# Optimization experiments

Hardware: AMD Instinct MI355X
Metric: run time of the kernel (lower is better)

## Reference

```python
import jax, jax.numpy as jnp
import numpy as np

F_FRAMES = 128   # number of frames (seq_start_end rows)
P_PEDS = 32      # pedestrians per frame (uniform)
B = F_FRAMES * P_PEDS
E, H, BN, PM, M = 64, 128, 1024, 512, 1024
PRED_LEN = 12


def setup_inputs() -> dict:
    key = jax.random.key(0)
    ks = jax.random.split(key, 20)
    n = lambda k, s, sc=0.05: (jax.random.normal(k, s) * sc).astype(jnp.float32)
    starts = jnp.arange(F_FRAMES, dtype=jnp.int32) * P_PEDS
    seq_start_end = jnp.stack([starts, starts + P_PEDS], axis=1)
    return {
        "h0": n(ks[0], (1, B, H), 1.0),
        "c0": n(ks[1], (1, B, H), 1.0),
        "obs_final_pos": n(ks[2], (B, 2), 1.0),
        "obs_final_pos_rel": n(ks[3], (B, 2), 1.0),
        "W_emb": n(ks[4], (2, E)), "b_emb": jnp.zeros((E,), jnp.float32),
        "W_ih": n(ks[5], (4 * H, E)), "W_hh": n(ks[6], (4 * H, H)),
        "b_ih": jnp.zeros((4 * H,), jnp.float32), "b_hh": jnp.zeros((4 * H,), jnp.float32),
        "W_pos": n(ks[7], (H, 2)), "b_pos": jnp.zeros((2,), jnp.float32),
        "W_pe": n(ks[8], (2, E)), "b_pe": jnp.zeros((E,), jnp.float32),
        "W_p1": n(ks[9], (E + H, PM)), "b_p1": jnp.zeros((PM,), jnp.float32),
        "W_p2": n(ks[10], (PM, BN)), "b_p2": jnp.zeros((BN,), jnp.float32),
        "W_m1": n(ks[11], (H + BN, M)), "b_m1": jnp.zeros((M,), jnp.float32),
        "W_m2": n(ks[12], (M, H)), "b_m2": jnp.zeros((H,), jnp.float32),
        "seq_start_end": seq_start_end,
    }


def reference(h0, c0, obs_final_pos, obs_final_pos_rel,
              W_emb, b_emb, W_ih, W_hh, b_ih, b_hh, W_pos, b_pos,
              W_pe, b_pe, W_p1, b_p1, W_p2, b_p2, W_m1, b_m1, W_m2, b_m2,
              seq_start_end):
    Bn = h0.shape[1]
    F = seq_start_end.shape[0]
    P = Bn // F  # uniform frame size
    h, c = h0[0], c0[0]
    x0 = obs_final_pos_rel @ W_emb + b_emb  # decoder input embedding

    def step(carry, _):
        x, h, c, last_pos = carry
        # LSTM cell (PyTorch gate order i,f,g,o)
        gates = x @ W_ih.T + h @ W_hh.T + b_ih + b_hh  # (B, 4H)
        i, f, g, o = jnp.split(gates, 4, axis=-1)
        i, f, o = jax.nn.sigmoid(i), jax.nn.sigmoid(f), jax.nn.sigmoid(o)
        c_new = f * c + i * jnp.tanh(g)
        h_new = o * jnp.tanh(c_new)
        rel_pos = h_new @ W_pos + b_pos
        curr_pos = rel_pos + last_pos
        # PoolNet: per-frame pairwise rel-pos embed + MLP + max over neighbours j
        pos = curr_pos.reshape(F, P, 2)
        hf = h_new.reshape(F, P, H)
        rel = pos[:, None, :, :] - pos[:, :, None, :]  # rel[f,i,j] = pos_j - pos_i
        e = rel @ W_pe + b_pe  # (F,P,P,E)
        feat = jnp.concatenate(
            [e, jnp.broadcast_to(hf[:, None], (F, P, P, H))], axis=-1)  # h of j
        z = jax.nn.relu(feat @ W_p1 + b_p1)
        z = jax.nn.relu(z @ W_p2 + b_p2)  # (F,P,P,BN)
        pool_h = z.max(axis=2).reshape(Bn, BN)
        # hidden refresh MLP
        mi = jnp.concatenate([h_new, pool_h], axis=-1)
        nh = jax.nn.relu(mi @ W_m1 + b_m1)
        nh = jax.nn.relu(nh @ W_m2 + b_m2)
        x_new = rel_pos @ W_emb + b_emb
        return (x_new, nh, c_new, curr_pos), (curr_pos, rel_pos)

    _, (pred_seq, pred_seq_rel) = jax.lax.scan(
        jax.checkpoint(step), (x0, h, c, obs_final_pos), None, length=PRED_LEN)
    return pred_seq, pred_seq_rel
```

## Files before the change

### kernel.cpp

```cpp
#include <hip/hip_runtime.h>

#define NB 4096
#define HD 128
#define ED 64
#define NF 128
#define NP 32
#define TSTEPS 12

typedef __attribute__((ext_vector_type(8))) short short8;
typedef __attribute__((ext_vector_type(8))) __bf16 bf16x8;
typedef __attribute__((ext_vector_type(8))) _Float16 f16x8;
typedef __attribute__((ext_vector_type(4))) float f32x4;

#define MFMA16(a, b, c) __builtin_amdgcn_mfma_f32_16x16x32_bf16((a), (b), (c), 0, 0, 0)
#define MFMAH(a, b, c)  __builtin_amdgcn_mfma_f32_16x16x32_f16((a), (b), (c), 0, 0, 0)

__device__ __forceinline__ unsigned short f2bf(float f) {
  unsigned int x = __float_as_uint(f);
  x += 0x7fffu + ((x >> 16) & 1u);
  return (unsigned short)(x >> 16);
}

__device__ __forceinline__ float sigm(float x) { return 1.0f / (1.0f + expf(-x)); }

__device__ __forceinline__ f16x8 relu8(f16x8 x) {
  return __builtin_elementwise_max(x, (f16x8)(_Float16)0);
}


__global__ __launch_bounds__(256) void k_transpose_bf(const float* __restrict__ W,
                                                      unsigned short* __restrict__ Wt,
                                                      int K, int N) {
  __shared__ float t[32][33];
  int nb = blockIdx.x * 32, kb = blockIdx.y * 32;
  int tx = threadIdx.x & 31, ty = threadIdx.x >> 5;
  #pragma unroll
  for (int r = 0; r < 32; r += 8)
    t[ty + r][tx] = W[(size_t)(kb + ty + r) * N + nb + tx];
  __syncthreads();
  #pragma unroll
  for (int r = 0; r < 32; r += 8)
    Wt[(size_t)(nb + ty + r) * K + kb + tx] = f2bf(t[tx][ty + r]);
}

__global__ __launch_bounds__(256) void k_pack_bfrag(const float* __restrict__ Wp2,
                                                    _Float16* __restrict__ Bf) {
  int U = blockIdx.x * 256 + threadIdx.x;
  int l = U & 63, cb = (U >> 6) & 63, ks = U >> 12;
  int col = cb * 16 + (l & 15);
  int k0 = ks * 32 + (l >> 4) * 8;
  f16x8 r;
  #pragma unroll
  for (int e = 0; e < 8; ++e) r[e] = (_Float16)Wp2[(size_t)(k0 + e) * 1024 + col];
  *(f16x8*)(Bf + (size_t)U * 8) = r;
}

__global__ __launch_bounds__(256) void k_pack_lstm_w(const float* __restrict__ Wih,
                                                     const float* __restrict__ Whh,
                                                     float* __restrict__ WihT,
                                                     float* __restrict__ WhhT) {
  int idx = blockIdx.x * 256 + threadIdx.x;
  if (idx < 64 * 512) { int k = idx >> 9, n = idx & 511; WihT[idx] = Wih[n * 64 + k]; }
  if (idx < 128 * 512) { int k = idx >> 9, n = idx & 511; WhhT[idx] = Whh[n * 128 + k]; }
}

__global__ __launch_bounds__(256) void k_pack_wpp(const float* __restrict__ Wpe,
                                                  const float* __restrict__ bpe,
                                                  const float* __restrict__ Wp1,
                                                  const float* __restrict__ bp1,
                                                  float* __restrict__ Wpp,
                                                  float* __restrict__ cvec) {
  int n = blockIdx.x * 256 + threadIdx.x;
  if (n >= 512) return;
  float s0 = 0.f, s1 = 0.f, sc = 0.f;
  for (int k = 0; k < 64; ++k) {
    float w = Wp1[k * 512 + n];
    s0 += Wpe[k] * w;
    s1 += Wpe[64 + k] * w;
    sc += bpe[k] * w;
  }
  Wpp[n * 2] = s0; Wpp[n * 2 + 1] = s1; cvec[n] = sc + bp1[n];
}

__global__ __launch_bounds__(256) void k_x0(const float* __restrict__ ofr,
                                            const float* __restrict__ Wemb,
                                            const float* __restrict__ bemb,
                                            float* __restrict__ x) {
  int idx = blockIdx.x * 256 + threadIdx.x;
  if (idx >= NB * ED) return;
  int row = idx >> 6, e = idx & 63;
  x[idx] = bemb[e] + ofr[row * 2] * Wemb[e] + ofr[row * 2 + 1] * Wemb[64 + e];
}


__global__ __launch_bounds__(256) void k12_lstm_uv(
    const float* __restrict__ x, const float* __restrict__ hin, const float* __restrict__ cin,
    const float* __restrict__ WihT, const float* __restrict__ WhhT,
    const float* __restrict__ bih, const float* __restrict__ bhh,
    const float* __restrict__ Wpos, const float* __restrict__ bpos,
    const float* __restrict__ Wemb, const float* __restrict__ bemb,
    const float* __restrict__ lastpos,
    const float* __restrict__ Wp1, const float* __restrict__ Wpp,
    const float* __restrict__ cvec,
    float* __restrict__ cout, unsigned short* __restrict__ mi,
    float* __restrict__ posout, float* __restrict__ xout,
    float* __restrict__ outc, float* __restrict__ outr,
    _Float16* __restrict__ u16, _Float16* __restrict__ v16) {
  __shared__ float xh[8][192];
  __shared__ float hnl[8][128];
  __shared__ float rp[8][2];
  __shared__ float cp[8][2];
  int tid = threadIdx.x;
  int r0 = blockIdx.x * 8;
  for (int idx = tid; idx < 8 * 192; idx += 256) {
    int r = idx / 192, k = idx % 192;
    xh[r][k] = (k < 64) ? x[(r0 + r) * 64 + k] : hin[(r0 + r) * 128 + (k - 64)];
  }
  __syncthreads();
  int j = tid & 127, rg = tid >> 7;
  float acc0[4], acc1[4], acc2[4], acc3[4];
  {
    float b0 = bih[j] + bhh[j];
    float b1 = bih[128 + j] + bhh[128 + j];
    float b2 = bih[256 + j] + bhh[256 + j];
    float b3 = bih[384 + j] + bhh[384 + j];
    #pragma unroll
    for (int r = 0; r < 4; ++r) { acc0[r] = b0; acc1[r] = b1; acc2[r] = b2; acc3[r] = b3; }
  }
  for (int k = 0; k < 64; ++k) {
    float w0 = WihT[k * 512 + j], w1 = WihT[k * 512 + 128 + j],
          w2 = WihT[k * 512 + 256 + j], w3 = WihT[k * 512 + 384 + j];
    #pragma unroll
    for (int r = 0; r < 4; ++r) {
      float xv = xh[rg * 4 + r][k];
      acc0[r] += w0 * xv; acc1[r] += w1 * xv; acc2[r] += w2 * xv; acc3[r] += w3 * xv;
    }
  }
  for (int k = 0; k < 128; ++k) {
    float w0 = WhhT[k * 512 + j], w1 = WhhT[k * 512 + 128 + j],
          w2 = WhhT[k * 512 + 256 + j], w3 = WhhT[k * 512 + 384 + j];
    #pragma unroll
    for (int r = 0; r < 4; ++r) {
      float hv = xh[rg * 4 + r][64 + k];
      acc0[r] += w0 * hv; acc1[r] += w1 * hv; acc2[r] += w2 * hv; acc3[r] += w3 * hv;
    }
  }
  #pragma unroll
  for (int r = 0; r < 4; ++r) {
    int row = r0 + rg * 4 + r;
    float ig = sigm(acc0[r]), fg = sigm(acc1[r]), gg = tanhf(acc2[r]), og = sigm(acc3[r]);
    float cn = fg * cin[row * 128 + j] + ig * gg;
    float hv = og * tanhf(cn);
    cout[row * 128 + j] = cn;
    mi[(size_t)row * 1152 + j] = f2bf(hv);
    hnl[rg * 4 + r][j] = hv;
  }
  __syncthreads();
  {
    int r = tid >> 5;
    int d = (tid >> 4) & 1;
    int l = tid & 15;
    float s = 0.f;
    #pragma unroll
    for (int k = l; k < 128; k += 16) s += hnl[r][k] * Wpos[k * 2 + d];
    s += __shfl_xor(s, 1);
    s += __shfl_xor(s, 2);
    s += __shfl_xor(s, 4);
    s += __shfl_xor(s, 8);
    if (l == 0) {
      int row = r0 + r;
      float rel = s + bpos[d];
      float cur = rel + lastpos[row * 2 + d];
      rp[r][d] = rel;
      cp[r][d] = cur;
      posout[row * 2 + d] = cur;
      outc[row * 2 + d] = cur;
      outr[row * 2 + d] = rel;
    }
  }
  __syncthreads();
  for (int idx = tid; idx < 8 * 64; idx += 256) {
    int r = idx >> 6, e = idx & 63;
    xout[(r0 + r) * 64 + e] = bemb[e] + rp[r][0] * Wemb[e] + rp[r][1] * Wemb[64 + e];
  }
  int n = tid, n2 = tid + 256;
  float aA[8], aB[8];
  #pragma unroll
  for (int r = 0; r < 8; ++r) { aA[r] = 0.f; aB[r] = 0.f; }
  for (int k = 0; k < 128; ++k) {
    float wA = Wp1[(64 + k) * 512 + n], wB = Wp1[(64 + k) * 512 + n2];
    #pragma unroll
    for (int r = 0; r < 8; ++r) { aA[r] += wA * hnl[r][k]; aB[r] += wB * hnl[r][k]; }
  }
  float wp0A = Wpp[n * 2], wp1A = Wpp[n * 2 + 1], cA = cvec[n];
  float wp0B = Wpp[n2 * 2], wp1B = Wpp[n2 * 2 + 1], cB = cvec[n2];
  #pragma unroll
  for (int r = 0; r < 8; ++r) {
    int row = r0 + r;
    float t0 = cp[r][0] * wp0A + cp[r][1] * wp1A;
    v16[(size_t)row * 512 + n] = (_Float16)t0;
    u16[(size_t)row * 512 + n] = (_Float16)(t0 + aA[r] + cA);
    float t1 = cp[r][0] * wp0B + cp[r][1] * wp1B;
    v16[(size_t)row * 512 + n2] = (_Float16)t1;
    u16[(size_t)row * 512 + n2] = (_Float16)(t1 + aB[r] + cB);
  }
}

__global__ __launch_bounds__(256, 2) void k3_pool(
    const _Float16* __restrict__ u16, const _Float16* __restrict__ v16,
    const _Float16* __restrict__ Bf, const float* __restrict__ bp2,
    unsigned short* __restrict__ mi) {
  __shared__ _Float16 u_lds[32 * 512];
  __shared__ _Float16 v_lds[4 * 512];
  int f = blockIdx.x, ig = blockIdx.y, ng = blockIdx.z;
  int tid = threadIdx.x, wid = tid >> 6, lane = tid & 63;
  int c = lane & 15, q = lane >> 4;
  int ip = wid >> 1, nh = wid & 1;

  const f16x8* Bfu = (const f16x8*)Bf;
  int cb0 = ng * 16 + nh * 8;

  f16x8 B0[8], B1[8];
  #pragma unroll
  for (int nt = 0; nt < 8; ++nt)
    B0[nt] = Bfu[(size_t)((cb0 + nt) * 64 + lane)];

  #pragma unroll
  for (int t = 0; t < 8; ++t) {
    int unit = tid + t * 256;
    int row = unit >> 6, seg = unit & 63;
    f16x8 val = *(const f16x8*)(u16 + (size_t)(f * 32 + row) * 512 + seg * 8);
    int byte = (row << 10) + (seg << 4);
    byte ^= (row & 7) << 4;
    *(f16x8*)((char*)u_lds + byte) = val;
  }
  {
    int row = tid >> 6, seg = tid & 63;
    *(f16x8*)(v_lds + (row << 9) + seg * 8) =
        *(const f16x8*)(v16 + (size_t)(f * 32 + ig * 4 + row) * 512 + seg * 8);
  }
  __syncthreads();

  f32x4 acc[2][2][8];
  #pragma unroll
  for (int a = 0; a < 2; ++a)
    #pragma unroll
    for (int b = 0; b < 2; ++b)
      #pragma unroll
      for (int n = 0; n < 8; ++n) acc[a][b][n] = (f32x4){0.f, 0.f, 0.f, 0.f};

  int ub0 = (c << 10) + (q << 4);
  int usw = (c & 7) << 4;
  const _Float16* vp0 = v_lds + ((ip * 2 + 0) << 9) + q * 8;
  const _Float16* vp1 = vp0 + 512;

  #pragma unroll
  for (int ks = 0; ks < 16; ++ks) {
    if (ks < 15) {
      #pragma unroll
      for (int nt = 0; nt < 8; ++nt)
        B1[nt] = Bfu[(size_t)(((ks + 1) * 64 + cb0 + nt) * 64 + lane)];
    }
    int kb = ks << 6;
    f16x8 uf0 = *(const f16x8*)((const char*)u_lds + ((ub0 + kb) ^ usw));
    f16x8 uf1 = *(const f16x8*)((const char*)u_lds + ((ub0 + 16384 + kb) ^ usw));
    f16x8 vv0 = *(const f16x8*)(vp0 + ks * 32);
    f16x8 vv1 = *(const f16x8*)(vp1 + ks * 32);
    f16x8 a00 = relu8(uf0 - vv0), a01 = relu8(uf1 - vv0);
    f16x8 a10 = relu8(uf0 - vv1), a11 = relu8(uf1 - vv1);
    __builtin_amdgcn_s_setprio(1);
    #pragma unroll
    for (int nt = 0; nt < 8; ++nt) {
      f16x8 bf = B0[nt];
      acc[0][0][nt] = MFMAH(a00, bf, acc[0][0][nt]);
      acc[0][1][nt] = MFMAH(a01, bf, acc[0][1][nt]);
      acc[1][0][nt] = MFMAH(a10, bf, acc[1][0][nt]);
      acc[1][1][nt] = MFMAH(a11, bf, acc[1][1][nt]);
    }
    __builtin_amdgcn_s_setprio(0);
    #pragma unroll
    for (int nt = 0; nt < 8; ++nt) B0[nt] = B1[nt];
  }

  int colbase = ng * 256 + nh * 128;
  #pragma unroll
  for (int ii = 0; ii < 2; ++ii) {
    int rowg = f * 32 + ig * 4 + ip * 2 + ii;
    #pragma unroll
    for (int nt = 0; nt < 8; ++nt) {
      f32x4 x0 = acc[ii][0][nt], x1 = acc[ii][1][nt];
      float m = fmaxf(fmaxf(fmaxf(x0[0], x0[1]), fmaxf(x0[2], x0[3])),
                      fmaxf(fmaxf(x1[0], x1[1]), fmaxf(x1[2], x1[3])));
      m = fmaxf(m, __shfl_xor(m, 16));
      m = fmaxf(m, __shfl_xor(m, 32));
      if (q == 0) {
        int col = colbase + nt * 16 + c;
        float val = fmaxf(m + bp2[col], 0.f);
        mi[(size_t)rowg * 1152 + 128 + col] = f2bf(val);
      }
    }
  }
}

__global__ __launch_bounds__(512) void k4_mlp1(
    const unsigned short* __restrict__ mi, const unsigned short* __restrict__ Wt,
    const float* __restrict__ bm1, unsigned short* __restrict__ nh1) {
  int bid = blockIdx.x;
  int mb = bid & 63, nb = bid >> 6;
  int tid = threadIdx.x, wid = tid >> 6, lane = tid & 63;
  int row0 = mb * 64 + (wid >> 2) * 32;
  int nc0 = nb * 256 + (wid & 3) * 64;
  int c = lane & 15, q = lane >> 4;
  const unsigned short* a0p = mi + (size_t)(row0 + c) * 1152;
  const unsigned short* a1p = a0p + 16 * 1152;
  const unsigned short* bb = Wt + (size_t)(nc0 + c) * 1152;
  f32x4 acc[2][4];
  #pragma unroll
  for (int a = 0; a < 2; ++a)
    #pragma unroll
    for (int b = 0; b < 4; ++b) acc[a][b] = (f32x4){0.f, 0.f, 0.f, 0.f};
  for (int ks = 0; ks < 36; ++ks) {
    int k0 = ks * 32 + q * 8;
    bf16x8 a0 = *(const bf16x8*)(a0p + k0);
    bf16x8 a1 = *(const bf16x8*)(a1p + k0);
    #pragma unroll
    for (int nt = 0; nt < 4; ++nt) {
      bf16x8 bf = *(const bf16x8*)(bb + (size_t)nt * 16 * 1152 + k0);
      acc[0][nt] = MFMA16(a0, bf, acc[0][nt]);
      acc[1][nt] = MFMA16(a1, bf, acc[1][nt]);
    }
  }
  #pragma unroll
  for (int mt = 0; mt < 2; ++mt)
    #pragma unroll
    for (int nt = 0; nt < 4; ++nt)
      #pragma unroll
      for (int r = 0; r < 4; ++r) {
        int row = row0 + mt * 16 + q * 4 + r;
        int col = nc0 + nt * 16 + c;
        float val = fmaxf(acc[mt][nt][r] + bm1[col], 0.f);
        nh1[(size_t)row * 1024 + col] = f2bf(val);
      }
}

__global__ __launch_bounds__(128) void k5_mlp2(
    const unsigned short* __restrict__ nh1, const unsigned short* __restrict__ Wt,
    const float* __restrict__ bm2, float* __restrict__ hout) {
  int bid = blockIdx.x;
  int tid = threadIdx.x, wid = tid >> 6, lane = tid & 63;
  int row0 = bid * 16;
  int nc0 = wid * 64;
  int c = lane & 15, q = lane >> 4;
  const unsigned short* ap = nh1 + (size_t)(row0 + c) * 1024;
  const unsigned short* bb = Wt + (size_t)(nc0 + c) * 1024;
  f32x4 acc[4];
  #pragma unroll
  for (int b = 0; b < 4; ++b) acc[b] = (f32x4){0.f, 0.f, 0.f, 0.f};
  for (int ks = 0; ks < 32; ++ks) {
    int k0 = ks * 32 + q * 8;
    bf16x8 a = *(const bf16x8*)(ap + k0);
    #pragma unroll
    for (int nt = 0; nt < 4; ++nt) {
      bf16x8 bf = *(const bf16x8*)(bb + (size_t)nt * 16 * 1024 + k0);
      acc[nt] = MFMA16(a, bf, acc[nt]);
    }
  }
  #pragma unroll
  for (int nt = 0; nt < 4; ++nt)
    #pragma unroll
    for (int r = 0; r < 4; ++r) {
      int row = row0 + q * 4 + r;
      int col = nc0 + nt * 16 + c;
      hout[(size_t)row * 128 + col] = fmaxf(acc[nt][r] + bm2[col], 0.f);
    }
}


extern "C" void kernel_launch(void* const* d_in, const int* in_sizes, int n_in,
                              void* d_out, int out_size, void* d_ws, size_t ws_size,
                              hipStream_t stream) {
  const float* h0   = (const float*)d_in[0];
  const float* c0   = (const float*)d_in[1];
  const float* ofp  = (const float*)d_in[2];
  const float* ofr  = (const float*)d_in[3];
  const float* Wemb = (const float*)d_in[4];
  const float* bemb = (const float*)d_in[5];
  const float* Wih  = (const float*)d_in[6];
  const float* Whh  = (const float*)d_in[7];
  const float* bih  = (const float*)d_in[8];
  const float* bhh  = (const float*)d_in[9];
  const float* Wpos = (const float*)d_in[10];
  const float* bpos = (const float*)d_in[11];
  const float* Wpe  = (const float*)d_in[12];
  const float* bpe  = (const float*)d_in[13];
  const float* Wp1  = (const float*)d_in[14];
  const float* bp1  = (const float*)d_in[15];
  const float* Wp2  = (const float*)d_in[16];
  const float* bp2  = (const float*)d_in[17];
  const float* Wm1  = (const float*)d_in[18];
  const float* bm1  = (const float*)d_in[19];
  const float* Wm2  = (const float*)d_in[20];
  const float* bm2  = (const float*)d_in[21];

  char* ws = (char*)d_ws;
  size_t off = 0;
  auto alloc = [&](size_t bytes) {
    char* p = ws + off;
    off += (bytes + 255) & ~(size_t)255;
    return p;
  };
  float* h    = (float*)alloc((size_t)NB * HD * 4);
  float* cst  = (float*)alloc((size_t)NB * HD * 4);
  float* xbuf = (float*)alloc((size_t)NB * ED * 4);
  float* pos  = (float*)alloc((size_t)NB * 2 * 4);
  _Float16* u16 = (_Float16*)alloc((size_t)NB * 512 * 2);
  _Float16* v16 = (_Float16*)alloc((size_t)NB * 512 * 2);
  unsigned short* mi   = (unsigned short*)alloc((size_t)NB * 1152 * 2);
  unsigned short* nh1  = (unsigned short*)alloc((size_t)NB * 1024 * 2);
  float* WihT = (float*)alloc(64 * 512 * 4);
  float* WhhT = (float*)alloc(128 * 512 * 4);
  float* Wpp  = (float*)alloc(512 * 2 * 4);
  float* cvec = (float*)alloc(512 * 4);
  _Float16* Bf  = (_Float16*)alloc((size_t)1024 * 512 * 2);
  unsigned short* Wm1t = (unsigned short*)alloc((size_t)1024 * 1152 * 2);
  unsigned short* Wm2t = (unsigned short*)alloc((size_t)128 * 1024 * 2);

  float* outc = (float*)d_out;
  float* outr = outc + (size_t)TSTEPS * NB * 2;

  k_pack_lstm_w<<<256, 256, 0, stream>>>(Wih, Whh, WihT, WhhT);
  k_pack_wpp<<<2, 256, 0, stream>>>(Wpe, bpe, Wp1, bp1, Wpp, cvec);
  k_pack_bfrag<<<256, 256, 0, stream>>>(Wp2, Bf);
  k_transpose_bf<<<dim3(1024 / 32, 1152 / 32), 256, 0, stream>>>(Wm1, Wm1t, 1152, 1024);
  k_transpose_bf<<<dim3(128 / 32, 1024 / 32), 256, 0, stream>>>(Wm2, Wm2t, 1024, 128);
  k_x0<<<NB * ED / 256, 256, 0, stream>>>(ofr, Wemb, bemb, xbuf);

  for (int t = 0; t < TSTEPS; ++t) {
    const float* hin = (t == 0) ? h0 : h;
    const float* cin = (t == 0) ? c0 : cst;
    const float* lp  = (t == 0) ? ofp : pos;
    k12_lstm_uv<<<NB / 8, 256, 0, stream>>>(xbuf, hin, cin, WihT, WhhT, bih, bhh,
                                            Wpos, bpos, Wemb, bemb, lp, Wp1, Wpp, cvec,
                                            cst, mi, pos, xbuf,
                                            outc + (size_t)t * NB * 2,
                                            outr + (size_t)t * NB * 2, u16, v16);
    k3_pool<<<dim3(128, 8, 4), 256, 0, stream>>>(u16, v16, Bf, bp2, mi);
    k4_mlp1<<<256, 512, 0, stream>>>(mi, Wm1t, bm1, nh1);
    k5_mlp2<<<256, 128, 0, stream>>>(nh1, Wm2t, bm2, h);
  }
}
```

Baseline: 2.723 ms.

## Switch pool kernel to 32x32x16 f16 MFMA with deeper B prefetch and block swizzle

Rewrites the pool GEMM to use 32x32x16 f16 MFMA instructions instead of 16x16x32, repacking Wp2 fragments to the matching layout. Each A fragment now covers all 32 neighbours, so only one u load and two relu subtracts are needed per k-step, and the max over neighbours is mostly done in registers. B fragments are prefetched two steps ahead through a four-slot rotating buffer. The grid becomes one-dimensional with a remapped block index so that consecutive blocks span different ng and ig groups, which is meant to improve cache locality for the shared B weights. The larger accumulator tiles and the extra buffering may raise register pressure.

Result: slower. 2.836 ms (+4.2%).

```diff
diff --git a/kernel.cpp b/kernel.cpp
--- a/kernel.cpp
+++ b/kernel.cpp
@@ -11,9 +11,10 @@
 typedef __attribute__((ext_vector_type(8))) __bf16 bf16x8;
 typedef __attribute__((ext_vector_type(8))) _Float16 f16x8;
 typedef __attribute__((ext_vector_type(4))) float f32x4;
-
-#define MFMA16(a, b, c) __builtin_amdgcn_mfma_f32_16x16x32_bf16((a), (b), (c), 0, 0, 0)
-#define MFMAH(a, b, c)  __builtin_amdgcn_mfma_f32_16x16x32_f16((a), (b), (c), 0, 0, 0)
+typedef __attribute__((ext_vector_type(16))) float f32x16;
+
+#define MFMA16(a, b, c)  __builtin_amdgcn_mfma_f32_16x16x32_bf16((a), (b), (c), 0, 0, 0)
+#define MFMA32H(a, b, c) __builtin_amdgcn_mfma_f32_32x32x16_f16((a), (b), (c), 0, 0, 0)
 
 __device__ __forceinline__ unsigned short f2bf(float f) {
   unsigned int x = __float_as_uint(f);
@@ -43,12 +44,12 @@
     Wt[(size_t)(nb + ty + r) * K + kb + tx] = f2bf(t[tx][ty + r]);
 }
 
-__global__ __launch_bounds__(256) void k_pack_bfrag(const float* __restrict__ Wp2,
-                                                    _Float16* __restrict__ Bf) {
+__global__ __launch_bounds__(256) void k_pack_bfrag32(const float* __restrict__ Wp2,
+                                                      _Float16* __restrict__ Bf) {
   int U = blockIdx.x * 256 + threadIdx.x;
-  int l = U & 63, cb = (U >> 6) & 63, ks = U >> 12;
-  int col = cb * 16 + (l & 15);
-  int k0 = ks * 32 + (l >> 4) * 8;
+  int l = U & 63, cb = (U >> 6) & 31, ks = U >> 11;
+  int col = cb * 32 + (l & 31);
+  int k0 = ks * 16 + (l >> 5) * 8;
   f16x8 r;
   #pragma unroll
   for (int e = 0; e < 8; ++e) r[e] = (_Float16)Wp2[(size_t)(k0 + e) * 1024 + col];
@@ -212,18 +213,20 @@
     unsigned short* __restrict__ mi) {
   __shared__ _Float16 u_lds[32 * 512];
   __shared__ _Float16 v_lds[4 * 512];
-  int f = blockIdx.x, ig = blockIdx.y, ng = blockIdx.z;
+  int bid = (blockIdx.x & 7) * 512 + (blockIdx.x >> 3);
+  int f = bid & 127, ig = (bid >> 7) & 7, ng = bid >> 10;
   int tid = threadIdx.x, wid = tid >> 6, lane = tid & 63;
-  int c = lane & 15, q = lane >> 4;
+  int r32 = lane & 31, hi = lane >> 5;
   int ip = wid >> 1, nh = wid & 1;
 
   const f16x8* Bfu = (const f16x8*)Bf;
-  int cb0 = ng * 16 + nh * 8;
-
-  f16x8 B0[8], B1[8];
-  #pragma unroll
-  for (int nt = 0; nt < 8; ++nt)
-    B0[nt] = Bfu[(size_t)((cb0 + nt) * 64 + lane)];
+  int cb0 = ng * 8 + nh * 4;
+
+  f16x8 Bb[4][4];
+  #pragma unroll
+  for (int nt = 0; nt < 4; ++nt) Bb[0][nt] = Bfu[(size_t)((0 * 32 + cb0 + nt) * 64 + lane)];
+  #pragma unroll
+  for (int nt = 0; nt < 4; ++nt) Bb[1][nt] = Bfu[(size_t)((1 * 32 + cb0 + nt) * 64 + lane)];
 
   #pragma unroll
   for (int t = 0; t < 8; ++t) {
@@ -241,60 +244,60 @@
   }
   __syncthreads();
 
-  f32x4 acc[2][2][8];
+  f32x16 acc[2][4];
   #pragma unroll
   for (int a = 0; a < 2; ++a)
     #pragma unroll
-    for (int b = 0; b < 2; ++b)
+    for (int n = 0; n < 4; ++n)
       #pragma unroll
-      for (int n = 0; n < 8; ++n) acc[a][b][n] = (f32x4){0.f, 0.f, 0.f, 0.f};
-
-  int ub0 = (c << 10) + (q << 4);
-  int usw = (c & 7) << 4;
-  const _Float16* vp0 = v_lds + ((ip * 2 + 0) << 9) + q * 8;
+      for (int r = 0; r < 16; ++r) acc[a][n][r] = 0.f;
+
+  int ubase = (r32 << 10) + (hi << 4);
+  int usw = (r32 & 7) << 4;
+  const _Float16* vp0 = v_lds + ((ip * 2 + 0) << 9) + hi * 8;
   const _Float16* vp1 = vp0 + 512;
 
-  #pragma unroll
-  for (int ks = 0; ks < 16; ++ks) {
-    if (ks < 15) {
-      #pragma unroll
-      for (int nt = 0; nt < 8; ++nt)
-        B1[nt] = Bfu[(size_t)(((ks + 1) * 64 + cb0 + nt) * 64 + lane)];
-    }
-    int kb = ks << 6;
-    f16x8 uf0 = *(const f16x8*)((const char*)u_lds + ((ub0 + kb) ^ usw));
-    f16x8 uf1 = *(const f16x8*)((const char*)u_lds + ((ub0 + 16384 + kb) ^ usw));
-    f16x8 vv0 = *(const f16x8*)(vp0 + ks * 32);
-    f16x8 vv1 = *(const f16x8*)(vp1 + ks * 32);
-    f16x8 a00 = relu8(uf0 - vv0), a01 = relu8(uf1 - vv0);
-    f16x8 a10 = relu8(uf0 - vv1), a11 = relu8(uf1 - vv1);
-    __builtin_amdgcn_s_setprio(1);
-    #pragma unroll
-    for (int nt = 0; nt < 8; ++nt) {
-      f16x8 bf = B0[nt];
-      acc[0][0][nt] = MFMAH(a00, bf, acc[0][0][nt]);
-      acc[0][1][nt] = MFMAH(a01, bf, acc[0][1][nt]);
-      acc[1][0][nt] = MFMAH(a10, bf, acc[1][0][nt]);
-      acc[1][1][nt] = MFMAH(a11, bf, acc[1][1][nt]);
-    }
-    __builtin_amdgcn_s_setprio(0);
-    #pragma unroll
-    for (int nt = 0; nt < 8; ++nt) B0[nt] = B1[nt];
-  }
-
-  int colbase = ng * 256 + nh * 128;
+#define K3STEP(KS, CUR, NXT, KLOAD)                                              \
+  {                                                                              \
+    if ((KLOAD) < 32) {                                                          \
+      _Pragma("unroll")                                                          \
+      for (int nt = 0; nt < 4; ++nt)                                             \
+        Bb[NXT][nt] = Bfu[(size_t)(((KLOAD) * 32 + cb0 + nt) * 64 + lane)];      \
+    }                                                                            \
+    f16x8 uf = *(const f16x8*)((const char*)u_lds + ((ubase + (KS) * 32) ^ usw));\
+    f16x8 vv0 = *(const f16x8*)(vp0 + (KS) * 16);                                \
+    f16x8 vv1 = *(const f16x8*)(vp1 + (KS) * 16);                                \
+    f16x8 a0 = relu8(uf - vv0);                                                  \
+    f16x8 a1 = relu8(uf - vv1);                                                  \
+    __builtin_amdgcn_s_setprio(1);                                               \
+    _Pragma("unroll")                                                            \
+    for (int nt = 0; nt < 4; ++nt) {                                             \
+      acc[0][nt] = MFMA32H(a0, Bb[CUR][nt], acc[0][nt]);                         \
+      acc[1][nt] = MFMA32H(a1, Bb[CUR][nt], acc[1][nt]);                         \
+    }                                                                            \
+    __builtin_amdgcn_s_setprio(0);                                               \
+  }
+
+  #pragma unroll
+  for (int kk = 0; kk < 32; kk += 4) {
+    K3STEP(kk + 0, 0, 2, kk + 2)
+    K3STEP(kk + 1, 1, 3, kk + 3)
+    K3STEP(kk + 2, 2, 0, kk + 4)
+    K3STEP(kk + 3, 3, 1, kk + 5)
+  }
+#undef K3STEP
+
   #pragma unroll
   for (int ii = 0; ii < 2; ++ii) {
     int rowg = f * 32 + ig * 4 + ip * 2 + ii;
     #pragma unroll
-    for (int nt = 0; nt < 8; ++nt) {
-      f32x4 x0 = acc[ii][0][nt], x1 = acc[ii][1][nt];
-      float m = fmaxf(fmaxf(fmaxf(x0[0], x0[1]), fmaxf(x0[2], x0[3])),
-                      fmaxf(fmaxf(x1[0], x1[1]), fmaxf(x1[2], x1[3])));
-      m = fmaxf(m, __shfl_xor(m, 16));
+    for (int nt = 0; nt < 4; ++nt) {
+      float m = acc[ii][nt][0];
+      #pragma unroll
+      for (int r = 1; r < 16; ++r) m = fmaxf(m, acc[ii][nt][r]);
       m = fmaxf(m, __shfl_xor(m, 32));
-      if (q == 0) {
-        int col = colbase + nt * 16 + c;
+      if (hi == 0) {
+        int col = (cb0 + nt) * 32 + r32;
         float val = fmaxf(m + bp2[col], 0.f);
         mi[(size_t)rowg * 1152 + 128 + col] = f2bf(val);
       }
@@ -430,7 +433,7 @@
 
   k_pack_lstm_w<<<256, 256, 0, stream>>>(Wih, Whh, WihT, WhhT);
   k_pack_wpp<<<2, 256, 0, stream>>>(Wpe, bpe, Wp1, bp1, Wpp, cvec);
-  k_pack_bfrag<<<256, 256, 0, stream>>>(Wp2, Bf);
+  k_pack_bfrag32<<<256, 256, 0, stream>>>(Wp2, Bf);
   k_transpose_bf<<<dim3(1024 / 32, 1152 / 32), 256, 0, stream>>>(Wm1, Wm1t, 1152, 1024);
   k_transpose_bf<<<dim3(128 / 32, 1024 / 32), 256, 0, stream>>>(Wm2, Wm2t, 1024, 128);
   k_x0<<<NB * ED / 256, 256, 0, stream>>>(ofr, Wemb, bemb, xbuf);
@@ -444,7 +447,7 @@
                                             cst, mi, pos, xbuf,
                                             outc + (size_t)t * NB * 2,
                                             outr + (size_t)t * NB * 2, u16, v16);
-    k3_pool<<<dim3(128, 8, 4), 256, 0, stream>>>(u16, v16, Bf, bp2, mi);
+    k3_pool<<<4096, 256, 0, stream>>>(u16, v16, Bf, bp2, mi);
     k4_mlp1<<<256, 512, 0, stream>>>(mi, Wm1t, bm1, nh1);
     k5_mlp2<<<256, 128, 0, stream>>>(nh1, Wm2t, bm2, h);
   }
```
